# Performance work log

Measured on AMD Instinct MI355X. Metric: run time of the kernel, lower is better.

Reference implementation:

```python
import jax, jax.numpy as jnp
import numpy as np

H = 128       # hidden
NRBF = 6
NSBF = 42
NB = 8        # n_bilinear
E = 131072    # edges
T = 1048576   # triplets

act = jax.nn.silu


def _lin(k, fan_in, shape):
    return jax.random.normal(k, shape, jnp.float32) * (1.0 / np.sqrt(fan_in))


def setup_inputs() -> dict:
    key = jax.random.key(0)
    ks = jax.random.split(key, 24)
    inp = {
        "m": jax.random.normal(ks[0], (E, H), jnp.float32),
        "rbf": jax.random.normal(ks[1], (E, NRBF), jnp.float32),
        "sbf": jax.random.normal(ks[2], (T, NSBF), jnp.float32),
        "edge_index": jax.random.randint(ks[3], (2, E), 0, E),
        "triplet_index": jax.random.randint(ks[4], (2, T), 0, E),
        # weights stored as [in, out] (torch Linear applies x @ W.T + b)
        "W_rbf": _lin(ks[5], NRBF, (NRBF, H)),
        "W_sbf": _lin(ks[6], NSBF, (NSBF, NB)),
        "W_kj": _lin(ks[7], H, (H, H)),
        "b_kj": jnp.zeros((H,), jnp.float32),
        "W_ji": _lin(ks[8], H, (H, H)),
        "b_ji": jnp.zeros((H,), jnp.float32),
        "W_bil": jax.random.normal(ks[9], (H, NB, H), jnp.float32) * 0.01,
        "r1_w1": _lin(ks[10], H, (H, H)), "r1_b1": jnp.zeros((H,), jnp.float32),
        "r1_w2": _lin(ks[11], H, (H, H)), "r1_b2": jnp.zeros((H,), jnp.float32),
        "r2_w1": _lin(ks[12], H, (H, H)), "r2_b1": jnp.zeros((H,), jnp.float32),
        "r2_w2": _lin(ks[13], H, (H, H)), "r2_b2": jnp.zeros((H,), jnp.float32),
        "W_out": _lin(ks[14], H, (H, H)), "b_out": jnp.zeros((H,), jnp.float32),
    }
    return inp


def _residual(x, w1, b1, w2, b2):
    h = act(act(x) @ w1 + b1)
    return x + h @ w2 + b2


def _forward(m, rbf, sbf, triplet_index,
             W_rbf, W_sbf, W_kj, b_kj, W_ji, b_ji, W_bil,
             r1_w1, r1_b1, r1_w2, r1_b2, r2_w1, r2_b1, r2_w2, r2_b2,
             W_out, b_out):
    kj_idx, ji_idx = triplet_index[0], triplet_index[1]

    x_ji = act(m @ W_ji + b_ji)                      # [E, H]

    m_kj = m[kj_idx]                                 # [T, H] gather
    x_kj = act(m_kj @ W_kj + b_kj) * (rbf[kj_idx] @ W_rbf)  # [T, H]

    sbf_proj = sbf @ W_sbf                           # [T, NB]
    # einsum('hbk,tb,th->tk') without materializing [T,H,H] or [T,NB,H]:
    # loop over the small fixed n_bilinear dim (8 GEMMs of [T,H]x[H,H]).
    msg = sbf_proj[:, 0:1] * (x_kj @ W_bil[:, 0, :])
    for b in range(1, NB):
        msg = msg + sbf_proj[:, b:b + 1] * (x_kj @ W_bil[:, b, :])

    aggr = jax.ops.segment_sum(msg, ji_idx, num_segments=m.shape[0])  # [E, H]

    m_new = x_ji + aggr
    m_new = _residual(m_new, r1_w1, r1_b1, r1_w2, r1_b2)
    m_new = _residual(m_new, r2_w1, r2_b1, r2_w2, r2_b2)
    m_new = act(m_new @ W_out + b_out)
    return m + m_new


def reference(m, rbf, sbf, edge_index, triplet_index,
              W_rbf, W_sbf, W_kj, b_kj, W_ji, b_ji, W_bil,
              r1_w1, r1_b1, r1_w2, r1_b2, r2_w1, r2_b1, r2_w2, r2_b2,
              W_out, b_out):
    # edge_index is accepted for signature parity but unused (as in the source).
    return _forward(m, rbf, sbf, triplet_index,
                    W_rbf, W_sbf, W_kj, b_kj, W_ji, b_ji, W_bil,
                    r1_w1, r1_b1, r1_w2, r1_b2, r2_w1, r2_b1, r2_w2, r2_b2,
                    W_out, b_out)
```

## Files before the change

kernel.cpp:

```cpp
#include <hip/hip_runtime.h>
#include <hip/hip_bf16.h>
#include <stdint.h>

typedef uint16_t u16;
typedef uint32_t u32;
typedef uint64_t u64;
typedef short bf16x8 __attribute__((ext_vector_type(8)));
typedef float f32x4 __attribute__((ext_vector_type(4)));
typedef u32 u32x4 __attribute__((ext_vector_type(4)));

#define E_N 131072
#define T_N 1048576

__device__ __forceinline__ float bf2f(u32 u) { return __builtin_bit_cast(float, u << 16); }
__device__ __forceinline__ u16 f2bf(float f) {
  u32 u = __builtin_bit_cast(u32, f);
  return (u16)((u + 0x7fffu + ((u >> 16) & 1u)) >> 16);
}
__device__ __forceinline__ float silu_f(float x) { return x / (1.0f + __expf(-x)); }
__device__ __forceinline__ f32x4 mfma16(bf16x8 a, bf16x8 b, f32x4 c) {
  return __builtin_amdgcn_mfma_f32_16x16x32_bf16(a, b, c, 0, 0, 0);
}
__device__ __forceinline__ void gld_lds16(const void* g, void* l) {
  __builtin_amdgcn_global_load_lds((const __attribute__((address_space(1))) u32*)g,
                                   (__attribute__((address_space(3))) u32*)l, 16, 0, 0);
}
#define WAIT_VM0() do { asm volatile("s_waitcnt vmcnt(0)" ::: "memory"); \
                        __builtin_amdgcn_sched_barrier(0); } while (0)

__device__ __forceinline__ bf16x8 ldfrag(const char* base, u32 tile, u32 ks, u32 lane) {
  return *(const bf16x8*)(base + (((tile << 2) + ks) << 10) + lane * 16);
}

__global__ __launch_bounds__(256) void k_init(
    const float* __restrict__ Wji, const float* __restrict__ Wkj, const float* __restrict__ Wbil,
    const float* __restrict__ w11, const float* __restrict__ w12,
    const float* __restrict__ w21, const float* __restrict__ w22, const float* __restrict__ wout,
    u16* __restrict__ dst, const int* __restrict__ trip, int* __restrict__ cnt) {
  u32 bid = blockIdx.x;
  if (bid >= 960) {
    u32 t = (bid - 960) * 256 + threadIdx.x;
    atomicAdd(&cnt[trip[T_N + t]], 1);
    return;
  }
  u32 idx = bid * 256 + threadIdx.x;
  if (idx >= 245760) return;
  float v;
  if (idx < 163840) {
    u32 j = idx & 7, lane = (idx >> 3) & 63, ks = (idx >> 9) & 3;
    u32 k = ((ks << 2) + (lane >> 4)) * 8 + j;
    u32 nl = lane & 15;
    if (idx < 32768) {
      u32 g = idx >> 11;
      u32 n = g * 16 + nl;
      v = (n < 128) ? Wji[k * 128 + n] : Wkj[k * 128 + (n - 128)];
    } else {
      u32 q = idx - 32768;
      u32 g = (q >> 11) & 7, b = q >> 14;
      v = Wbil[k * 1024 + b * 128 + g * 16 + nl];
    }
  } else {
    u32 q = idx - 163840;
    u32 r = q >> 14, n = (q >> 7) & 127, h = q & 127;
    const float* src = (r == 0) ? w11 : (r == 1) ? w12 : (r == 2) ? w21 : (r == 3) ? w22 : wout;
    v = src[h * 128 + n];
  }
  dst[idx] = f2bf(v);
}

__global__ __launch_bounds__(256) void k_scanA(const int* __restrict__ cnt,
                                               int* __restrict__ offsA, int* __restrict__ blksum) {
  __shared__ int s[256];
  u32 b = blockIdx.x, tid = threadIdx.x;
  int v = cnt[b * 256 + tid];
  s[tid] = v; __syncthreads();
  for (int d = 1; d < 256; d <<= 1) {
    int t = (tid >= (u32)d) ? s[tid - d] : 0;
    __syncthreads(); s[tid] += t; __syncthreads();
  }
  offsA[b * 256 + tid] = s[tid] - v;
  if (tid == 255) blksum[b] = s[255];
}
__global__ __launch_bounds__(512) void k_scanB(const int* __restrict__ blksum, int* __restrict__ blkoff) {
  __shared__ int s[512];
  u32 tid = threadIdx.x;
  int v = blksum[tid];
  s[tid] = v; __syncthreads();
  for (int d = 1; d < 512; d <<= 1) {
    int t = (tid >= (u32)d) ? s[tid - d] : 0;
    __syncthreads(); s[tid] += t; __syncthreads();
  }
  blkoff[tid] = s[tid] - v;
}
__global__ __launch_bounds__(256) void k_scanC(const int* __restrict__ offsA,
                                               const int* __restrict__ blkoff, int* __restrict__ offs_work) {
  u32 i = blockIdx.x * 256 + threadIdx.x;
  offs_work[i] = offsA[i] + blkoff[blockIdx.x];
}

__global__ __launch_bounds__(512) void k_mid(
    const float* __restrict__ m, const float* __restrict__ rbf, const float* __restrict__ Wrbf,
    const float* __restrict__ bkj, const float* __restrict__ bji,
    const char* __restrict__ W2F, float* __restrict__ aggr, u16* __restrict__ ek,
    const int* __restrict__ trip, const float* __restrict__ sbf, const float* __restrict__ Wsbf,
    int* __restrict__ offs_work, char* __restrict__ srec) {
  const u32 tid = threadIdx.x;
  if (blockIdx.x >= 1024) {
    u32 t = (blockIdx.x - 1024) * 512 + tid;
    int kj = trip[t], ji = trip[T_N + t];
    int p = atomicAdd(&offs_work[ji], 1);
    float o[8] = {0.f, 0.f, 0.f, 0.f, 0.f, 0.f, 0.f, 0.f};
    const float* sr = sbf + (size_t)t * 42;
#pragma unroll
    for (int q = 0; q < 42; ++q) {
      float r = sr[q];
#pragma unroll
      for (int c = 0; c < 8; ++c) o[c] += r * Wsbf[q * 8 + c];
    }
    u32x4 r0, r1;
    r0[0] = (u32)kj; r0[1] = (u32)ji;
    r0[2] = (u32)f2bf(o[0]) | ((u32)f2bf(o[1]) << 16);
    r0[3] = (u32)f2bf(o[2]) | ((u32)f2bf(o[3]) << 16);
    r1[0] = (u32)f2bf(o[4]) | ((u32)f2bf(o[5]) << 16);
    r1[1] = (u32)f2bf(o[6]) | ((u32)f2bf(o[7]) << 16);
    r1[2] = 0; r1[3] = 0;
    *(u32x4*)(srec + (size_t)p * 32) = r0;
    *(u32x4*)(srec + (size_t)p * 32 + 16) = r1;
    return;
  }
  extern __shared__ char lds[];
  char* ldsA = lds;
  float* ldsRbf = (float*)(lds + 32768);
  float* ldsWr = (float*)(lds + 35840);
  const u32 lane = tid & 63;
  const u32 r0_ = blockIdx.x << 7;

#pragma unroll
  for (int it = 0; it < 8; ++it) {
    u32 q = tid + it * 512;
    u32 row = q >> 5, c4 = q & 31;
    f32x4 v = *(const f32x4*)(m + (size_t)(r0_ + row) * 128 + c4 * 4);
    u32 c = c4 >> 1, half = c4 & 1;
    u32 w0 = (u32)f2bf(v[0]) | ((u32)f2bf(v[1]) << 16);
    u32 w1 = (u32)f2bf(v[2]) | ((u32)f2bf(v[3]) << 16);
    u32 ofs = (row << 8) + ((c ^ (row & 7)) << 4) + half * 8;
    *(u64*)(ldsA + ofs) = (u64)w0 | ((u64)w1 << 32);
  }
  for (u32 i = tid; i < 768; i += 512) ldsRbf[i] = rbf[(size_t)r0_ * 6 + i];
  for (u32 i = tid; i < 768; i += 512) ldsWr[i] = Wrbf[i];
  __syncthreads();

  const u32 wid = tid >> 6, wm = wid >> 2, wn = wid & 3;
  const u32 rb = wm << 6, cb = wn << 6;
  f32x4 acc[4][4] = {};
  bf16x8 Bf[4][4];
#pragma unroll
  for (int ni = 0; ni < 4; ++ni)
#pragma unroll
    for (int ks = 0; ks < 4; ++ks) Bf[ni][ks] = ldfrag(W2F, wn * 4 + ni, ks, lane);
#pragma unroll
  for (int mi = 0; mi < 4; ++mi) {
    u32 row = rb + mi * 16 + (lane & 15);
    bf16x8 Af[4];
#pragma unroll
    for (int ks = 0; ks < 4; ++ks)
      Af[ks] = *(const bf16x8*)(ldsA + (row << 8) + ((((u32)(ks * 4) + (lane >> 4)) ^ (row & 7)) << 4));
#pragma unroll
    for (int ni = 0; ni < 4; ++ni)
#pragma unroll
      for (int ks = 0; ks < 4; ++ks) acc[mi][ni] = mfma16(Af[ks], Bf[ni][ks], acc[mi][ni]);
  }
#pragma unroll
  for (int mi = 0; mi < 4; ++mi) {
    u32 rloc = rb + mi * 16 + ((lane >> 4) << 2);
#pragma unroll
    for (int j = 0; j < 4; ++j) {
      u32 rl = rloc + j;
      size_t grow = r0_ + rl;
#pragma unroll
      for (int ni = 0; ni < 4; ++ni) {
        u32 col = cb + ni * 16 + (lane & 15);
        float v = acc[mi][ni][j];
        if (col < 128) {
          aggr[grow * 128 + col] = silu_f(v + bji[col]);
        } else {
          u32 c2 = col - 128;
          float rw = 0.f;
#pragma unroll
          for (int q = 0; q < 6; ++q) rw += ldsRbf[rl * 6 + q] * ldsWr[q * 128 + c2];
          ek[grow * 128 + c2] = f2bf(silu_f(v + bkj[c2]) * rw);
        }
      }
    }
  }
}

__global__ __launch_bounds__(256, 2) void k_bil(
    const char* __restrict__ ek, const char* __restrict__ srec,
    const char* __restrict__ WF, float* __restrict__ aggr) {
  extern __shared__ char lds[];
  char* Xl = lds;
  u16* msg16 = (u16*)lds;
  float* spT = (float*)(lds + 32768);
  int* jil = (int*)(lds + 36864);
  int* kjl = (int*)(lds + 37376);
  int* rstart = (int*)(lds + 37888);
  int* scnt = (int*)(lds + 38400);
  const u32 tid = threadIdx.x, lane = tid & 63, wid = tid >> 6;
  const u32 wm = wid >> 1, wn = wid & 1, rb = wm << 6, cb = wn << 6;
  const u32 t0 = blockIdx.x << 7;

  if (tid < 128) {
    const char* rp = srec + (size_t)(t0 + tid) * 32;
    u32x4 a = *(const u32x4*)rp;
    u32 c0 = *(const u32*)(rp + 16);
    u32 c1 = *(const u32*)(rp + 20);
    kjl[tid] = (int)a[0];
    jil[tid] = (int)a[1];
    spT[0 * 128 + tid] = bf2f(a[2] & 0xffffu);
    spT[1 * 128 + tid] = bf2f(a[2] >> 16);
    spT[2 * 128 + tid] = bf2f(a[3] & 0xffffu);
    spT[3 * 128 + tid] = bf2f(a[3] >> 16);
    spT[4 * 128 + tid] = bf2f(c0 & 0xffffu);
    spT[5 * 128 + tid] = bf2f(c0 >> 16);
    spT[6 * 128 + tid] = bf2f(c1 & 0xffffu);
    spT[7 * 128 + tid] = bf2f(c1 >> 16);
  }
  __syncthreads();

#pragma unroll
  for (int it = 0; it < 8; ++it) {
    u32 q = tid + it * 256, row = q >> 4, c = q & 15;
    gld_lds16(ek + (size_t)kjl[row] * 256 + ((c ^ (row & 7)) << 4), Xl + q * 16);
  }
  int isS = 0;
  u32 pre = 0;
  if (tid < 128) {
    isS = (tid == 0) || (jil[tid] != jil[tid - 1]);
    u64 mask = __ballot(isS);
    pre = (u32)__popcll(mask & ((1ull << lane) - 1ull));
    if (lane == 0) scnt[wid] = (int)__popcll(mask);
  }
  WAIT_VM0();
  __syncthreads();
  if (tid < 128 && isS) {
    u32 off = (wid == 1) ? (u32)scnt[0] : 0u;
    rstart[pre + off] = (int)tid;
  }

  bf16x8 Afr[4][4];
#pragma unroll
  for (int mi = 0; mi < 4; ++mi) {
    u32 row = rb + mi * 16 + (lane & 15);
#pragma unroll
    for (int ks = 0; ks < 4; ++ks)
      Afr[mi][ks] = *(const bf16x8*)(Xl + (row << 8) + ((((u32)(ks * 4) + (lane >> 4)) ^ (row & 7)) << 4));
  }
  __syncthreads();

  f32x4 acc[4][4] = {};
  for (int b = 0; b < 8; ++b) {
    const char* wb = WF + (size_t)b * 32768;
    bf16x8 Bf[4][4];
#pragma unroll
    for (int ni = 0; ni < 4; ++ni)
#pragma unroll
      for (int ks = 0; ks < 4; ++ks) Bf[ni][ks] = ldfrag(wb, wn * 4 + ni, ks, lane);
#pragma unroll
    for (int mi = 0; mi < 4; ++mi) {
      f32x4 s4 = *(const f32x4*)(spT + b * 128 + rb + mi * 16 + ((lane >> 4) << 2));
#pragma unroll
      for (int ni = 0; ni < 4; ++ni) {
        f32x4 p = {0.f, 0.f, 0.f, 0.f};
#pragma unroll
        for (int ks = 0; ks < 4; ++ks) p = mfma16(Afr[mi][ks], Bf[ni][ks], p);
        acc[mi][ni] += s4 * p;
      }
    }
  }

#pragma unroll
  for (int mi = 0; mi < 4; ++mi) {
    u32 rloc = rb + mi * 16 + ((lane >> 4) << 2);
#pragma unroll
    for (int j = 0; j < 4; ++j) {
      u16* drow = msg16 + (size_t)(rloc + j) * 128 + cb + (lane & 15);
#pragma unroll
      for (int ni = 0; ni < 4; ++ni) drow[ni * 16] = f2bf(acc[mi][ni][j]);
    }
  }
  __syncthreads();

  const u32 nr = (u32)(scnt[0] + scnt[1]);
  for (u32 task = tid; task < nr * 128; task += 256) {
    u32 run = task >> 7, col = task & 127;
    int ra = rstart[run];
    int rz = (run + 1 < nr) ? rstart[run + 1] : 128;
    float s = 0.f;
    for (int r = ra; r < rz; ++r) s += bf2f(msg16[(size_t)r * 128 + col]);
    unsafeAtomicAdd(&aggr[(size_t)jil[ra] * 128 + col], s);
  }
}

__global__ __launch_bounds__(256, 2) void k_res(
    const float* __restrict__ aggr, const float* __restrict__ m,
    const char* __restrict__ rT,
    const float* __restrict__ rb1, const float* __restrict__ rb2,
    const float* __restrict__ rb3, const float* __restrict__ rb4,
    const float* __restrict__ bo, float* __restrict__ out) {
  extern __shared__ char lds[];
  char* ldsA = lds;
  char* ldsB = lds + 32768;
  const u32 tid = threadIdx.x, lane = tid & 63, wid = tid >> 6;
  const u32 r0 = blockIdx.x << 7;
  const u32 wm = wid >> 1, wn = wid & 1, rbw = wm << 6, cbw = wn << 6;
  const u32 lrow = (lane >> 4) << 2, lcol = lane & 15;

  auto stageB = [&](const char* WT) {
#pragma unroll
    for (int it = 0; it < 8; ++it) {
      u32 q = tid + it * 256, n = q >> 4, c = q & 15;
      gld_lds16(WT + n * 256 + ((c ^ (n & 7)) << 4), ldsB + q * 16);
    }
  };
  auto writeA = [&](u32 row, u32 col, float v) {
    *(u16*)(ldsA + (row << 8) + ((((col >> 3)) ^ (row & 7)) << 4) + (col & 7) * 2) = f2bf(v);
  };
  auto compute = [&](f32x4 (&acc)[4][4]) {
#pragma unroll
    for (int mi = 0; mi < 4; ++mi) {
      u32 row = rbw + mi * 16 + lcol;
      bf16x8 Af[4];
#pragma unroll
      for (int ks = 0; ks < 4; ++ks)
        Af[ks] = *(const bf16x8*)(ldsA + (row << 8) + ((((u32)(ks * 4) + (lane >> 4)) ^ (row & 7)) << 4));
#pragma unroll
      for (int ni = 0; ni < 4; ++ni) {
        u32 n = cbw + ni * 16 + lcol;
#pragma unroll
        for (int ks = 0; ks < 4; ++ks) {
          bf16x8 Bk = *(const bf16x8*)(ldsB + (n << 8) + ((((u32)(ks * 4) + (lane >> 4)) ^ (n & 7)) << 4));
          acc[mi][ni] = mfma16(Af[ks], Bk, acc[mi][ni]);
        }
      }
    }
  };
  auto zero = [&](f32x4 (&acc)[4][4]) {
#pragma unroll
    for (int a = 0; a < 4; ++a)
#pragma unroll
      for (int c = 0; c < 4; ++c) acc[a][c] = (f32x4){0.f, 0.f, 0.f, 0.f};
  };

  f32x4 xr[4][4];
#pragma unroll
  for (int mi = 0; mi < 4; ++mi)
#pragma unroll
    for (int j = 0; j < 4; ++j) {
      const float* src = aggr + (size_t)(r0 + rbw + mi * 16 + lrow + j) * 128 + cbw + lcol;
#pragma unroll
      for (int ni = 0; ni < 4; ++ni) xr[mi][ni][j] = src[ni * 16];
    }
  stageB(rT);
#pragma unroll
  for (int mi = 0; mi < 4; ++mi)
#pragma unroll
    for (int j = 0; j < 4; ++j) {
      u32 row = rbw + mi * 16 + lrow + j;
#pragma unroll
      for (int ni = 0; ni < 4; ++ni) writeA(row, cbw + ni * 16 + lcol, silu_f(xr[mi][ni][j]));
    }
  __syncthreads();

  f32x4 acc[4][4];
  zero(acc); compute(acc);
  __syncthreads();
#pragma unroll
  for (int mi = 0; mi < 4; ++mi)
#pragma unroll
    for (int j = 0; j < 4; ++j) {
      u32 row = rbw + mi * 16 + lrow + j;
#pragma unroll
      for (int ni = 0; ni < 4; ++ni) {
        u32 col = cbw + ni * 16 + lcol;
        writeA(row, col, silu_f(acc[mi][ni][j] + rb1[col]));
      }
    }
  stageB(rT + 32768);
  __syncthreads();

  zero(acc); compute(acc);
  __syncthreads();
#pragma unroll
  for (int mi = 0; mi < 4; ++mi)
#pragma unroll
    for (int j = 0; j < 4; ++j) {
      u32 row = rbw + mi * 16 + lrow + j;
#pragma unroll
      for (int ni = 0; ni < 4; ++ni) {
        u32 col = cbw + ni * 16 + lcol;
        xr[mi][ni][j] += acc[mi][ni][j] + rb2[col];
        writeA(row, col, silu_f(xr[mi][ni][j]));
      }
    }
  stageB(rT + 65536);
  __syncthreads();

  zero(acc); compute(acc);
  __syncthreads();
#pragma unroll
  for (int mi = 0; mi < 4; ++mi)
#pragma unroll
    for (int j = 0; j < 4; ++j) {
      u32 row = rbw + mi * 16 + lrow + j;
#pragma unroll
      for (int ni = 0; ni < 4; ++ni) {
        u32 col = cbw + ni * 16 + lcol;
        writeA(row, col, silu_f(acc[mi][ni][j] + rb3[col]));
      }
    }
  stageB(rT + 98304);
  __syncthreads();

  zero(acc); compute(acc);
  __syncthreads();
#pragma unroll
  for (int mi = 0; mi < 4; ++mi)
#pragma unroll
    for (int j = 0; j < 4; ++j) {
      u32 row = rbw + mi * 16 + lrow + j;
#pragma unroll
      for (int ni = 0; ni < 4; ++ni) {
        u32 col = cbw + ni * 16 + lcol;
        xr[mi][ni][j] += acc[mi][ni][j] + rb4[col];
        writeA(row, col, xr[mi][ni][j]);
      }
    }
  stageB(rT + 131072);
#pragma unroll
  for (int mi = 0; mi < 4; ++mi)
#pragma unroll
    for (int j = 0; j < 4; ++j) {
      const float* src = m + (size_t)(r0 + rbw + mi * 16 + lrow + j) * 128 + cbw + lcol;
#pragma unroll
      for (int ni = 0; ni < 4; ++ni) xr[mi][ni][j] = src[ni * 16];
    }
  __syncthreads();

  zero(acc); compute(acc);
#pragma unroll
  for (int mi = 0; mi < 4; ++mi)
#pragma unroll
    for (int j = 0; j < 4; ++j) {
      size_t grow = r0 + rbw + mi * 16 + lrow + j;
#pragma unroll
      for (int ni = 0; ni < 4; ++ni) {
        u32 col = cbw + ni * 16 + lcol;
        out[grow * 128 + col] = xr[mi][ni][j] + silu_f(acc[mi][ni][j] + bo[col]);
      }
    }
}

extern "C" void kernel_launch(void* const* d_in, const int* in_sizes, int n_in,
                              void* d_out, int out_size, void* d_ws, size_t ws_size,
                              hipStream_t stream) {
  const float* m = (const float*)d_in[0];
  const float* rbf = (const float*)d_in[1];
  const float* sbf = (const float*)d_in[2];
  const int* trip = (const int*)d_in[4];
  const float* Wrbf = (const float*)d_in[5];
  const float* Wsbf = (const float*)d_in[6];
  const float* bkj = (const float*)d_in[8];
  const float* bji = (const float*)d_in[10];
  const float* r1b1 = (const float*)d_in[13];
  const float* r1b2 = (const float*)d_in[15];
  const float* r2b1 = (const float*)d_in[17];
  const float* r2b2 = (const float*)d_in[19];
  const float* bout = (const float*)d_in[21];

  char* ws = (char*)d_ws;
  char* W2F = ws;
  char* WF = ws + 65536;
  char* rT = ws + 327680;
  u16* ek = (u16*)(ws + 524288);
  char* srec = ws + 34078720;
  float* aggr = (float*)(ws + 67633152);
  int* cnt = (int*)(ws + 134742016);
  int* offsA = (int*)(ws + 135266304);
  int* blksum = (int*)(ws + 135790592);
  int* blkoff = (int*)(ws + 135792640);
  int* offs_work = (int*)(ws + 135794688);

  hipFuncSetAttribute((const void*)k_mid, hipFuncAttributeMaxDynamicSharedMemorySize, 38912);
  hipFuncSetAttribute((const void*)k_bil, hipFuncAttributeMaxDynamicSharedMemorySize, 38912);
  hipFuncSetAttribute((const void*)k_res, hipFuncAttributeMaxDynamicSharedMemorySize, 65536);

  hipMemsetAsync(cnt, 0, 131072 * sizeof(int), stream);
  k_init<<<5056, 256, 0, stream>>>(
      (const float*)d_in[9], (const float*)d_in[7], (const float*)d_in[11],
      (const float*)d_in[12], (const float*)d_in[14], (const float*)d_in[16],
      (const float*)d_in[18], (const float*)d_in[20], (u16*)ws, trip, cnt);
  k_scanA<<<512, 256, 0, stream>>>(cnt, offsA, blksum);
  k_scanB<<<1, 512, 0, stream>>>(blksum, blkoff);
  k_scanC<<<512, 256, 0, stream>>>(offsA, blkoff, offs_work);
  k_mid<<<3072, 512, 38912, stream>>>(m, rbf, Wrbf, bkj, bji, W2F, aggr, ek,
                                      trip, sbf, Wsbf, offs_work, srec);
  k_bil<<<8192, 256, 38912, stream>>>((const char*)ek, (const char*)srec, WF, aggr);
  k_res<<<1024, 256, 65536, stream>>>(aggr, m, rT, r1b1, r1b2, r2b1, r2b2, bout,
                                      (float*)d_out);
}
```

Measured before the change: 782.9 us.

## Fold block-offset scan into scanC, vectorize sbf loads, halve k_res row tile

Removes the single-block k_scanB launch: each k_scanC block now reduces the preceding block sums itself to get its offset. The sbf projection loop reads sbf two floats at a time. k_res processes 64 rows per block instead of 128, using 48KB of LDS across 2048 blocks. The smaller tile cuts registers and LDS per block, allowing more blocks per CU, but each weight tile is staged twice as often per row.

Result: faster. 646.7 us (-17.4%).

```diff
diff --git a/kernel.cpp b/kernel.cpp
--- a/kernel.cpp
+++ b/kernel.cpp
@@ -6,6 +6,7 @@
 typedef uint32_t u32;
 typedef uint64_t u64;
 typedef short bf16x8 __attribute__((ext_vector_type(8)));
+typedef float f32x2 __attribute__((ext_vector_type(2)));
 typedef float f32x4 __attribute__((ext_vector_type(4)));
 typedef u32 u32x4 __attribute__((ext_vector_type(4)));
 
@@ -81,21 +82,20 @@
   offsA[b * 256 + tid] = s[tid] - v;
   if (tid == 255) blksum[b] = s[255];
 }
-__global__ __launch_bounds__(512) void k_scanB(const int* __restrict__ blksum, int* __restrict__ blkoff) {
-  __shared__ int s[512];
-  u32 tid = threadIdx.x;
-  int v = blksum[tid];
-  s[tid] = v; __syncthreads();
-  for (int d = 1; d < 512; d <<= 1) {
-    int t = (tid >= (u32)d) ? s[tid - d] : 0;
-    __syncthreads(); s[tid] += t; __syncthreads();
-  }
-  blkoff[tid] = s[tid] - v;
-}
 __global__ __launch_bounds__(256) void k_scanC(const int* __restrict__ offsA,
-                                               const int* __restrict__ blkoff, int* __restrict__ offs_work) {
-  u32 i = blockIdx.x * 256 + threadIdx.x;
-  offs_work[i] = offsA[i] + blkoff[blockIdx.x];
+                                               const int* __restrict__ blksum,
+                                               int* __restrict__ offs_work) {
+  __shared__ int red[256];
+  u32 bid = blockIdx.x, tid = threadIdx.x;
+  int v = 0;
+  if (tid < bid) v = blksum[tid];
+  if (tid + 256 < bid) v += blksum[tid + 256];
+  red[tid] = v; __syncthreads();
+  for (int d = 128; d > 0; d >>= 1) {
+    if (tid < (u32)d) red[tid] += red[tid + d];
+    __syncthreads();
+  }
+  offs_work[bid * 256 + tid] = offsA[bid * 256 + tid] + red[0];
 }
 
 __global__ __launch_bounds__(512) void k_mid(
@@ -112,10 +112,11 @@
     float o[8] = {0.f, 0.f, 0.f, 0.f, 0.f, 0.f, 0.f, 0.f};
     const float* sr = sbf + (size_t)t * 42;
 #pragma unroll
-    for (int q = 0; q < 42; ++q) {
-      float r = sr[q];
-#pragma unroll
-      for (int c = 0; c < 8; ++c) o[c] += r * Wsbf[q * 8 + c];
+    for (int q2 = 0; q2 < 21; ++q2) {
+      f32x2 rv = *(const f32x2*)(sr + q2 * 2);
+      const float* w0 = Wsbf + (q2 * 2) * 8;
+#pragma unroll
+      for (int c = 0; c < 8; ++c) o[c] += rv[0] * w0[c] + rv[1] * w0[8 + c];
     }
     u32x4 r0, r1;
     r0[0] = (u32)kj; r0[1] = (u32)ji;
@@ -310,10 +311,10 @@
     const float* __restrict__ bo, float* __restrict__ out) {
   extern __shared__ char lds[];
   char* ldsA = lds;
-  char* ldsB = lds + 32768;
+  char* ldsB = lds + 16384;
   const u32 tid = threadIdx.x, lane = tid & 63, wid = tid >> 6;
-  const u32 r0 = blockIdx.x << 7;
-  const u32 wm = wid >> 1, wn = wid & 1, rbw = wm << 6, cbw = wn << 6;
+  const u32 r0 = blockIdx.x << 6;
+  const u32 wm = wid >> 1, wn = wid & 1, rbw = wm << 5, cbw = wn << 6;
   const u32 lrow = (lane >> 4) << 2, lcol = lane & 15;
 
   auto stageB = [&](const char* WT) {
@@ -326,9 +327,9 @@
   auto writeA = [&](u32 row, u32 col, float v) {
     *(u16*)(ldsA + (row << 8) + ((((col >> 3)) ^ (row & 7)) << 4) + (col & 7) * 2) = f2bf(v);
   };
-  auto compute = [&](f32x4 (&acc)[4][4]) {
-#pragma unroll
-    for (int mi = 0; mi < 4; ++mi) {
+  auto compute = [&](f32x4 (&acc)[2][4]) {
+#pragma unroll
+    for (int mi = 0; mi < 2; ++mi) {
       u32 row = rbw + mi * 16 + lcol;
       bf16x8 Af[4];
 #pragma unroll
@@ -345,16 +346,16 @@
       }
     }
   };
-  auto zero = [&](f32x4 (&acc)[4][4]) {
-#pragma unroll
-    for (int a = 0; a < 4; ++a)
+  auto zero = [&](f32x4 (&acc)[2][4]) {
+#pragma unroll
+    for (int a = 0; a < 2; ++a)
 #pragma unroll
       for (int c = 0; c < 4; ++c) acc[a][c] = (f32x4){0.f, 0.f, 0.f, 0.f};
   };
 
-  f32x4 xr[4][4];
-#pragma unroll
-  for (int mi = 0; mi < 4; ++mi)
+  f32x4 xr[2][4];
+#pragma unroll
+  for (int mi = 0; mi < 2; ++mi)
 #pragma unroll
     for (int j = 0; j < 4; ++j) {
       const float* src = aggr + (size_t)(r0 + rbw + mi * 16 + lrow + j) * 128 + cbw + lcol;
@@ -363,7 +364,7 @@
     }
   stageB(rT);
 #pragma unroll
-  for (int mi = 0; mi < 4; ++mi)
+  for (int mi = 0; mi < 2; ++mi)
 #pragma unroll
     for (int j = 0; j < 4; ++j) {
       u32 row = rbw + mi * 16 + lrow + j;
@@ -372,11 +373,11 @@
     }
   __syncthreads();
 
-  f32x4 acc[4][4];
+  f32x4 acc[2][4];
   zero(acc); compute(acc);
   __syncthreads();
 #pragma unroll
-  for (int mi = 0; mi < 4; ++mi)
+  for (int mi = 0; mi < 2; ++mi)
 #pragma unroll
     for (int j = 0; j < 4; ++j) {
       u32 row = rbw + mi * 16 + lrow + j;
@@ -392,7 +393,7 @@
   zero(acc); compute(acc);
   __syncthreads();
 #pragma unroll
-  for (int mi = 0; mi < 4; ++mi)
+  for (int mi = 0; mi < 2; ++mi)
 #pragma unroll
     for (int j = 0; j < 4; ++j) {
       u32 row = rbw + mi * 16 + lrow + j;
@@ -409,7 +410,7 @@
   zero(acc); compute(acc);
   __syncthreads();
 #pragma unroll
-  for (int mi = 0; mi < 4; ++mi)
+  for (int mi = 0; mi < 2; ++mi)
 #pragma unroll
     for (int j = 0; j < 4; ++j) {
       u32 row = rbw + mi * 16 + lrow + j;
@@ -425,7 +426,7 @@
   zero(acc); compute(acc);
   __syncthreads();
 #pragma unroll
-  for (int mi = 0; mi < 4; ++mi)
+  for (int mi = 0; mi < 2; ++mi)
 #pragma unroll
     for (int j = 0; j < 4; ++j) {
       u32 row = rbw + mi * 16 + lrow + j;
@@ -438,7 +439,7 @@
     }
   stageB(rT + 131072);
 #pragma unroll
-  for (int mi = 0; mi < 4; ++mi)
+  for (int mi = 0; mi < 2; ++mi)
 #pragma unroll
     for (int j = 0; j < 4; ++j) {
       const float* src = m + (size_t)(r0 + rbw + mi * 16 + lrow + j) * 128 + cbw + lcol;
@@ -449,7 +450,7 @@
 
   zero(acc); compute(acc);
 #pragma unroll
-  for (int mi = 0; mi < 4; ++mi)
+  for (int mi = 0; mi < 2; ++mi)
 #pragma unroll
     for (int j = 0; j < 4; ++j) {
       size_t grow = r0 + rbw + mi * 16 + lrow + j;
@@ -488,12 +489,11 @@
   int* cnt = (int*)(ws + 134742016);
   int* offsA = (int*)(ws + 135266304);
   int* blksum = (int*)(ws + 135790592);
-  int* blkoff = (int*)(ws + 135792640);
   int* offs_work = (int*)(ws + 135794688);
 
   hipFuncSetAttribute((const void*)k_mid, hipFuncAttributeMaxDynamicSharedMemorySize, 38912);
   hipFuncSetAttribute((const void*)k_bil, hipFuncAttributeMaxDynamicSharedMemorySize, 38912);
-  hipFuncSetAttribute((const void*)k_res, hipFuncAttributeMaxDynamicSharedMemorySize, 65536);
+  hipFuncSetAttribute((const void*)k_res, hipFuncAttributeMaxDynamicSharedMemorySize, 49152);
 
   hipMemsetAsync(cnt, 0, 131072 * sizeof(int), stream);
   k_init<<<5056, 256, 0, stream>>>(
@@ -501,11 +501,10 @@
       (const float*)d_in[12], (const float*)d_in[14], (const float*)d_in[16],
       (const float*)d_in[18], (const float*)d_in[20], (u16*)ws, trip, cnt);
   k_scanA<<<512, 256, 0, stream>>>(cnt, offsA, blksum);
-  k_scanB<<<1, 512, 0, stream>>>(blksum, blkoff);
-  k_scanC<<<512, 256, 0, stream>>>(offsA, blkoff, offs_work);
+  k_scanC<<<512, 256, 0, stream>>>(offsA, blksum, offs_work);
   k_mid<<<3072, 512, 38912, stream>>>(m, rbf, Wrbf, bkj, bji, W2F, aggr, ek,
                                       trip, sbf, Wsbf, offs_work, srec);
   k_bil<<<8192, 256, 38912, stream>>>((const char*)ek, (const char*)srec, WF, aggr);
-  k_res<<<1024, 256, 65536, stream>>>(aggr, m, rT, r1b1, r1b2, r2b1, r2b2, bout,
+  k_res<<<2048, 256, 49152, stream>>>(aggr, m, rT, r1b1, r1b2, r2b1, r2b2, bout,
                                       (float*)d_out);
 }
```
